# Optimization experiments

Hardware: AMD Instinct MI355X
Metric: run time of the kernel (lower is better)

## Reference

```python
import jax, jax.numpy as jnp
import numpy as np
import math

D = 1024
H = 16

def setup_inputs() -> dict:
    key = jax.random.key(0)
    ks = jax.random.split(key, 8)
    N, X, T = 2, 1024, 4096
    s = 1.0 / math.sqrt(D)
    return {
        "previous_output": jax.random.normal(ks[0], (N, X, D), jnp.float32),
        "context": jax.random.normal(ks[1], (N, T, D), jnp.float32),
        "Wq": jax.random.normal(ks[2], (D, D), jnp.float32) * s,
        "bq": jnp.zeros((D,), jnp.float32),
        "Wk": jax.random.normal(ks[3], (D, D), jnp.float32) * s,
        "bk": jnp.zeros((D,), jnp.float32),
        "Wv": jax.random.normal(ks[4], (D, D), jnp.float32) * s,
        "bv": jnp.zeros((D,), jnp.float32),
    }

def reference(previous_output, context, Wq, bq, Wk, bk, Wv, bv):
    N, X, _ = previous_output.shape
    T = context.shape[1]
    hd = D // H
    # linear projections (torch Linear: x @ W.T + b)
    q = (previous_output @ Wq.T + bq).reshape(N, X, H, hd).transpose(0, 2, 1, 3)  # (N,H,X,hd)
    k = (context @ Wk.T + bk).reshape(N, T, H, hd).transpose(0, 2, 1, 3)          # (N,H,T,hd)
    v = (context @ Wv.T + bv).reshape(N, T, H, hd).transpose(0, 2, 1, 3)          # (N,H,T,hd)
    scores = jnp.einsum('nhxd,nhtd->nhxt', q, k) / jnp.sqrt(jnp.float32(hd))       # (N,H,X,T)
    attn = jax.nn.softmax(scores, axis=-1)
    out = jnp.einsum('nhxt,nhtd->nhxd', attn, v)                                   # (N,H,X,hd)
    return out.transpose(0, 2, 1, 3).reshape(N, X, D)
```

## Files before the change

kernel.cpp:

```cpp
#include <hip/hip_runtime.h>

typedef __bf16 bf16_t;
typedef __bf16 bf16x8 __attribute__((ext_vector_type(8)));
typedef __bf16 bf16x4 __attribute__((ext_vector_type(4)));
typedef float f32x4 __attribute__((ext_vector_type(4)));

#define D_MODEL 1024
#define NHEAD 16
#define HD 64
#define XLEN 1024
#define TLEN 4096
#define NBATCH 2
#define CEXP 0.18033688011112042f

typedef __attribute__((address_space(3))) bf16_t lds_bf16;
typedef const __attribute__((address_space(1))) bf16_t glb_bf16;

#define MEMFENCE() asm volatile("" ::: "memory")

__global__ __launch_bounds__(256) void convert5(const float* __restrict__ prev, const float* __restrict__ ctx,
                                                const float* __restrict__ wq, const float* __restrict__ wk,
                                                const float* __restrict__ wv,
                                                bf16_t* __restrict__ prev_b, bf16_t* __restrict__ ctx_b,
                                                bf16_t* __restrict__ wq_b, bf16_t* __restrict__ wk_b,
                                                bf16_t* __restrict__ wv_b) {
    int b = blockIdx.x;
    const float* src; bf16_t* dst; int lb;
    if (b < 256)       { src = prev; dst = prev_b; lb = b; }
    else if (b < 1280) { src = ctx;  dst = ctx_b;  lb = b - 256; }
    else if (b < 1408) { src = wq;   dst = wq_b;   lb = b - 1280; }
    else if (b < 1536) { src = wk;   dst = wk_b;   lb = b - 1408; }
    else               { src = wv;   dst = wv_b;   lb = b - 1536; }
    const int base = lb * 8192 + threadIdx.x * 4;
#pragma unroll
    for (int i = 0; i < 8; ++i) {
        const int off = base + i * 1024;
        f32x4 f = *(const f32x4*)(src + off);
        bf16x4 h;
        h[0] = (bf16_t)f[0]; h[1] = (bf16_t)f[1]; h[2] = (bf16_t)f[2]; h[3] = (bf16_t)f[3];
        *(bf16x4*)(dst + off) = h;
    }
}

template<int MF>
__device__ __forceinline__ void gemm_core(const bf16_t* __restrict__ Xa,
                                          const bf16_t* __restrict__ Wb,
                                          int m0, int n0, char* smem,
                                          f32x4 (&acc)[MF][4]) {
    const int tid  = threadIdx.x;
    const int w    = tid >> 6;
    const int lane = tid & 63;
    const int q4   = lane >> 4;
    const int c    = lane & 15;
    const int wm   = w >> 2;
    const int wn   = w & 3;

    constexpr int ABYTES = MF * 4096;
    constexpr int BUFSZ  = ABYTES + 32768;
    constexpr int AI     = MF / 4;
    constexpr int NT     = 16;

#pragma unroll
    for (int i = 0; i < MF; ++i)
#pragma unroll
        for (int j = 0; j < 4; ++j) acc[i][j] = (f32x4){0.f, 0.f, 0.f, 0.f};

    const int xp = ((lane & 3) * 16) ^ (((lane >> 5) & 1) << 5);
    const char* gA = (const char*)Xa + ((size_t)(m0 + w * 16 + (lane >> 2)) << 11) + xp;
    const char* gB = (const char*)Wb + ((size_t)(n0 + w * 16 + (lane >> 2)) << 11) + xp;
    char* lw = smem + w * 1024;

    const int fo = c * 64 + ((q4 * 16) ^ (((c >> 3) & 1) << 5));

#pragma unroll
    for (int i = 0; i < AI; ++i)
#pragma unroll
        for (int k = 0; k < 2; ++k)
            __builtin_amdgcn_global_load_lds((glb_bf16*)(gA + (size_t)i * 262144 + k * 64),
                                             (lds_bf16*)(lw + k * (MF * 2048) + i * 8192), 16, 0, 0);
#pragma unroll
    for (int i = 0; i < 2; ++i)
#pragma unroll
        for (int k = 0; k < 2; ++k)
            __builtin_amdgcn_global_load_lds((glb_bf16*)(gB + (size_t)i * 262144 + k * 64),
                                             (lds_bf16*)(lw + ABYTES + k * 16384 + i * 8192), 16, 0, 0);
    MEMFENCE();

#pragma unroll 1
    for (int t = 0; t < NT; ++t) {
        asm volatile("s_waitcnt vmcnt(0)" ::: "memory");
        __builtin_amdgcn_s_barrier();
        MEMFENCE();

        if (t + 1 < NT) {
            char* pb = lw + ((t + 1) & 1) * BUFSZ;
            const size_t tk = (size_t)(t + 1) * 128;
#pragma unroll
            for (int i = 0; i < AI; ++i)
#pragma unroll
                for (int k = 0; k < 2; ++k)
                    __builtin_amdgcn_global_load_lds((glb_bf16*)(gA + (size_t)i * 262144 + tk + k * 64),
                                                     (lds_bf16*)(pb + k * (MF * 2048) + i * 8192), 16, 0, 0);
#pragma unroll
            for (int i = 0; i < 2; ++i)
#pragma unroll
                for (int k = 0; k < 2; ++k)
                    __builtin_amdgcn_global_load_lds((glb_bf16*)(gB + (size_t)i * 262144 + tk + k * 64),
                                                     (lds_bf16*)(pb + ABYTES + k * 16384 + i * 8192), 16, 0, 0);
        }

        const char* cb = smem + (t & 1) * BUFSZ;
#pragma unroll
        for (int kk = 0; kk < 2; ++kk) {
            bf16x8 bfrag[4];
#pragma unroll
            for (int ni = 0; ni < 4; ++ni)
                bfrag[ni] = *(const bf16x8*)(cb + ABYTES + kk * 16384 + (wn * 4 + ni) * 1024 + fo);
            bf16x8 afrag[MF / 2];
#pragma unroll
            for (int mi = 0; mi < MF / 2; ++mi)
                afrag[mi] = *(const bf16x8*)(cb + kk * (MF * 2048) + (wm * MF + mi) * 1024 + fo);
            __builtin_amdgcn_s_setprio(1);
#pragma unroll
            for (int mi = 0; mi < MF / 2; ++mi)
#pragma unroll
                for (int ni = 0; ni < 4; ++ni)
                    acc[mi][ni] = __builtin_amdgcn_mfma_f32_16x16x32_bf16(afrag[mi], bfrag[ni], acc[mi][ni], 0, 0, 0);
            __builtin_amdgcn_s_setprio(0);

            bf16x8 afrag2[MF / 2];
#pragma unroll
            for (int mi = 0; mi < MF / 2; ++mi)
                afrag2[mi] = *(const bf16x8*)(cb + kk * (MF * 2048) + (wm * MF + MF / 2 + mi) * 1024 + fo);
            __builtin_amdgcn_s_setprio(1);
#pragma unroll
            for (int mi = 0; mi < MF / 2; ++mi)
#pragma unroll
                for (int ni = 0; ni < 4; ++ni)
                    acc[MF / 2 + mi][ni] = __builtin_amdgcn_mfma_f32_16x16x32_bf16(afrag2[mi], bfrag[ni], acc[MF / 2 + mi][ni], 0, 0, 0);
            __builtin_amdgcn_s_setprio(0);
            MEMFENCE();
        }
    }
}

__global__ __launch_bounds__(512, 2) void gemm_fused2(
    const bf16_t* __restrict__ Xq, const bf16_t* __restrict__ Xc,
    const bf16_t* __restrict__ wq, const bf16_t* __restrict__ wk, const bf16_t* __restrict__ wv,
    const float* __restrict__ bq, const float* __restrict__ bk, const float* __restrict__ bv,
    bf16_t* __restrict__ Qh, bf16_t* __restrict__ Kh, bf16_t* __restrict__ Vt) {
    __shared__ __align__(16) char smem[131072];
    const int bid  = blockIdx.x;
    const int tid  = threadIdx.x;
    const int w    = tid >> 6;
    const int lane = tid & 63;
    const int q4   = lane >> 4;
    const int c    = lane & 15;
    const int wm   = w >> 2;
    const int wn   = w & 3;
    (void)w;

    if (bid >= 64) {
        const int b     = bid - 64;
        const int r     = b & 7;
        const int j     = (b >> 3) & 7;
        const int mhi   = b >> 6;
        const int vmode = j >> 2;
        const int n0    = (j & 3) * 256;
        const int m0    = (mhi * 8 + r) * 256;
        const bf16_t* W   = vmode ? wv : wk;
        const float* bias = vmode ? bv : bk;

        const int Nw = n0 + wn * 64;
        float bz[4];
#pragma unroll
        for (int ni = 0; ni < 4; ++ni) bz[ni] = bias[Nw + ni * 16 + c];
        MEMFENCE();

        f32x4 acc[8][4];
        gemm_core<8>(Xc, W, m0, n0, smem, acc);

        const int Mw = m0 + wm * 128;
        const int headbase = Nw >> 6;
        if (vmode == 0) {
#pragma unroll
            for (int mi = 0; mi < 8; ++mi) {
                const int mrow = Mw + mi * 16 + q4 * 4;
                const int nb2 = mrow >> 12, pos = mrow & 4095;
                bf16_t* ob = Kh + ((size_t)(nb2 * NHEAD + headbase) * TLEN + pos) * HD;
#pragma unroll
                for (int ni = 0; ni < 4; ++ni) {
                    const int d = ni * 16 + c;
#pragma unroll
                    for (int r2 = 0; r2 < 4; ++r2)
                        ob[(size_t)r2 * HD + d] = (bf16_t)(acc[mi][ni][r2] + bz[ni]);
                }
            }
        } else {
#pragma unroll
            for (int mi = 0; mi < 8; ++mi) {
                const int mrow = Mw + mi * 16 + q4 * 4;
                const int nb2 = mrow >> 12, pos = mrow & 4095;
                const int lin = (pos & ~31) + ((pos >> 2) & 3) * 8 + ((pos >> 4) & 1) * 4;
#pragma unroll
                for (int ni = 0; ni < 4; ++ni) {
                    const int d = ni * 16 + c;
                    bf16x4 v4;
#pragma unroll
                    for (int r2 = 0; r2 < 4; ++r2) v4[r2] = (bf16_t)(acc[mi][ni][r2] + bz[ni]);
                    *(bf16x4*)(Vt + ((size_t)(nb2 * NHEAD + headbase) * HD + d) * TLEN + lin) = v4;
                }
            }
        }
    } else {
        const int b  = bid;
        const int m0 = (b >> 2) * 128;
        const int n0 = (b & 3) * 256;

        const int Nw = n0 + wn * 64;
        float bz[4];
#pragma unroll
        for (int ni = 0; ni < 4; ++ni) bz[ni] = bq[Nw + ni * 16 + c];
        MEMFENCE();

        f32x4 acc[4][4];
        gemm_core<4>(Xq, wq, m0, n0, smem, acc);

        const int Mw = m0 + wm * 64;
        const int headbase = Nw >> 6;
#pragma unroll
        for (int mi = 0; mi < 4; ++mi) {
            const int mrow = Mw + mi * 16 + q4 * 4;
            const int nb2 = mrow >> 10, pos = mrow & 1023;
            bf16_t* ob = Qh + ((size_t)(nb2 * NHEAD + headbase) * XLEN + pos) * HD;
#pragma unroll
            for (int ni = 0; ni < 4; ++ni) {
                const int d = ni * 16 + c;
#pragma unroll
                for (int r2 = 0; r2 < 4; ++r2)
                    ob[(size_t)r2 * HD + d] = (bf16_t)((acc[mi][ni][r2] + bz[ni]) * CEXP);
            }
        }
    }
}

__global__ __launch_bounds__(256, 4) void attn_kernel(const bf16_t* __restrict__ Qh,
                                                      const bf16_t* __restrict__ Kh,
                                                      const bf16_t* __restrict__ Vt,
                                                      bf16_t* __restrict__ Opart,
                                                      float* __restrict__ Lpart) {
    __shared__ __align__(16) char smem[32768];

    const int tid  = threadIdx.x;
    const int lane = tid & 63;
    const int w    = tid >> 6;
    const int q4   = lane >> 4;
    const int c    = lane & 15;

    const int bid = blockIdx.x;
    const int xcd = bid & 7;
    const int seq = bid >> 3;
    const int tq  = seq & 3;
    const int xb  = (seq >> 2) & 7;
    const int g   = seq >> 5;
    const int nh  = g * 8 + xcd;
    const int xw  = xb * 128 + w * 32;

    const bf16_t* __restrict__ Kb = Kh + (size_t)nh * TLEN * HD;
    const bf16_t* __restrict__ Vb = Vt + (size_t)nh * HD * TLEN;

    bf16x8 qa[2][2];
#pragma unroll
    for (int mi = 0; mi < 2; ++mi) {
        const bf16_t* qr = Qh + ((size_t)nh * XLEN + xw + mi * 16 + c) * HD + q4 * 8;
        qa[mi][0] = *(const bf16x8*)(qr);
        qa[mi][1] = *(const bf16x8*)(qr + 32);
    }

    const int sRow0 = tid >> 3,  sRow1 = 32 + (tid >> 3);
    const int sCh   = tid & 7;
    const int kCol0 = ((sCh ^ (sRow0 & 7)) * 8);
    const int kCol1 = ((sCh ^ (sRow1 & 7)) * 8);

    const int ofs0 = c * 128 + ((q4 ^ (c & 7)) * 16);
    const int ofs1 = c * 128 + (((4 + q4) ^ (c & 7)) * 16);

    f32x4 o[2][4];
#pragma unroll
    for (int i = 0; i < 2; ++i)
#pragma unroll
        for (int j = 0; j < 4; ++j) o[i][j] = (f32x4){0.f, 0.f, 0.f, 0.f};
    f32x4 lacc[2];
    lacc[0] = (f32x4){0.f, 0.f, 0.f, 0.f};
    lacc[1] = (f32x4){0.f, 0.f, 0.f, 0.f};

    bf16x8 ones8;
#pragma unroll
    for (int j = 0; j < 8; ++j) ones8[j] = (bf16_t)1.0f;

    const int t0base = tq * (TLEN / 4);

    {
        bf16_t* base = (bf16_t*)smem;
        __builtin_amdgcn_global_load_lds((glb_bf16*)(Kb + (size_t)(t0base + sRow0) * HD + kCol0), (lds_bf16*)(base + w * 512), 16, 0, 0);
        __builtin_amdgcn_global_load_lds((glb_bf16*)(Kb + (size_t)(t0base + sRow1) * HD + kCol1), (lds_bf16*)(base + 2048 + w * 512), 16, 0, 0);
        __builtin_amdgcn_global_load_lds((glb_bf16*)(Vb + (size_t)sRow0 * TLEN + t0base + kCol0), (lds_bf16*)(base + 4096 + w * 512), 16, 0, 0);
        __builtin_amdgcn_global_load_lds((glb_bf16*)(Vb + (size_t)sRow1 * TLEN + t0base + kCol1), (lds_bf16*)(base + 6144 + w * 512), 16, 0, 0);
    }

    for (int s = 0; s < 16; ++s) {
        __syncthreads();
        if (s < 15) {
            const int t1 = t0base + (s + 1) * 64;
            bf16_t* base = (bf16_t*)smem + ((s + 1) & 1) * 8192;
            __builtin_amdgcn_global_load_lds((glb_bf16*)(Kb + (size_t)(t1 + sRow0) * HD + kCol0), (lds_bf16*)(base + w * 512), 16, 0, 0);
            __builtin_amdgcn_global_load_lds((glb_bf16*)(Kb + (size_t)(t1 + sRow1) * HD + kCol1), (lds_bf16*)(base + 2048 + w * 512), 16, 0, 0);
            __builtin_amdgcn_global_load_lds((glb_bf16*)(Vb + (size_t)sRow0 * TLEN + t1 + kCol0), (lds_bf16*)(base + 4096 + w * 512), 16, 0, 0);
            __builtin_amdgcn_global_load_lds((glb_bf16*)(Vb + (size_t)sRow1 * TLEN + t1 + kCol1), (lds_bf16*)(base + 6144 + w * 512), 16, 0, 0);
        }

        const char* KtB = smem + (s & 1) * 16384;
        const char* VsB = KtB + 8192;
#pragma unroll
        for (int g32 = 0; g32 < 2; ++g32) {
            bf16x8 p8[2];
#pragma unroll
            for (int tt = 0; tt < 2; ++tt) {
                const int rofs = g32 * 4096 + tt * 2048;
                bf16x8 kb0 = *(const bf16x8*)(KtB + rofs + ofs0);
                bf16x8 kb1 = *(const bf16x8*)(KtB + rofs + ofs1);
#pragma unroll
                for (int mi = 0; mi < 2; ++mi) {
                    f32x4 sv = (f32x4){0.f, 0.f, 0.f, 0.f};
                    sv = __builtin_amdgcn_mfma_f32_16x16x32_bf16(kb0, qa[mi][0], sv, 0, 0, 0);
                    sv = __builtin_amdgcn_mfma_f32_16x16x32_bf16(kb1, qa[mi][1], sv, 0, 0, 0);
#pragma unroll
                    for (int r = 0; r < 4; ++r)
                        p8[mi][tt * 4 + r] = (bf16_t)__builtin_exp2f(sv[r]);
                }
            }
            const int vsel = g32 ? ofs1 : ofs0;
            bf16x8 va[4];
#pragma unroll
            for (int dt = 0; dt < 4; ++dt)
                va[dt] = *(const bf16x8*)(VsB + vsel + dt * 2048);
#pragma unroll
            for (int mi = 0; mi < 2; ++mi) {
#pragma unroll
                for (int dt = 0; dt < 4; ++dt)
                    o[mi][dt] = __builtin_amdgcn_mfma_f32_16x16x32_bf16(va[dt], p8[mi], o[mi][dt], 0, 0, 0);
                lacc[mi] = __builtin_amdgcn_mfma_f32_16x16x32_bf16(ones8, p8[mi], lacc[mi], 0, 0, 0);
            }
        }
    }

    __syncthreads();
    bf16_t* Ob = (bf16_t*)smem;
    float*  Lb = (float*)(smem + 16896);
#pragma unroll
    for (int mi = 0; mi < 2; ++mi) {
        if (q4 == 0) Lb[w * 32 + mi * 16 + c] = lacc[mi][0];
#pragma unroll
        for (int dt = 0; dt < 4; ++dt)
#pragma unroll
            for (int r = 0; r < 4; ++r)
                Ob[w * 2112 + (dt * 16 + q4 * 4 + r) * 33 + mi * 16 + c] = (bf16_t)o[mi][dt][r];
    }
    {
        const int lr = lane >> 1;
        const int dh = lane & 1;
        bf16x8 out4[4];
#pragma unroll
        for (int j2 = 0; j2 < 4; ++j2)
#pragma unroll
            for (int e = 0; e < 8; ++e)
                out4[j2][e] = Ob[w * 2112 + (dh * 32 + j2 * 8 + e) * 33 + lr];
        const size_t pair = (size_t)nh * XLEN + xw + lr;
        bf16_t* op = Opart + (pair * 4 + tq) * HD + dh * 32;
#pragma unroll
        for (int j2 = 0; j2 < 4; ++j2)
            *(bf16x8*)(op + j2 * 8) = out4[j2];
        if (dh == 0) Lpart[pair * 4 + tq] = Lb[w * 32 + lr];
    }
}

__global__ __launch_bounds__(256) void attn_merge(const bf16_t* __restrict__ Opart,
                                                  const float* __restrict__ Lpart,
                                                  float* __restrict__ Out) {
    const int u    = blockIdx.x * 256 + threadIdx.x;
    const int pair = u >> 3;
    const int d0   = (u & 7) * 8;
    const int nh   = pair >> 10;
    const int x    = pair & 1023;
    const int n    = nh >> 4;
    const int h    = nh & 15;

    float l = 0.f;
    float s[8];
#pragma unroll
    for (int j = 0; j < 8; ++j) s[j] = 0.f;
#pragma unroll
    for (int tqi = 0; tqi < 4; ++tqi) {
        l += Lpart[pair * 4 + tqi];
        bf16x8 v = *(const bf16x8*)(Opart + ((size_t)pair * 4 + tqi) * HD + d0);
#pragma unroll
        for (int j = 0; j < 8; ++j) s[j] += (float)v[j];
    }
    const float inv = 1.0f / l;
    f32x4 v0, v1;
#pragma unroll
    for (int j = 0; j < 4; ++j) { v0[j] = s[j] * inv; v1[j] = s[4 + j] * inv; }
    float* op = Out + ((size_t)(n * XLEN + x)) * D_MODEL + h * HD + d0;
    *(f32x4*)(op)     = v0;
    *(f32x4*)(op + 4) = v1;
}

extern "C" void kernel_launch(void* const* d_in, const int* in_sizes, int n_in,
                              void* d_out, int out_size, void* d_ws, size_t ws_size,
                              hipStream_t stream) {
    (void)in_sizes; (void)n_in; (void)out_size; (void)ws_size;
    const float* prev = (const float*)d_in[0];
    const float* ctx  = (const float*)d_in[1];
    const float* Wq   = (const float*)d_in[2];
    const float* bq   = (const float*)d_in[3];
    const float* Wk   = (const float*)d_in[4];
    const float* bk   = (const float*)d_in[5];
    const float* Wv   = (const float*)d_in[6];
    const float* bv   = (const float*)d_in[7];

    const size_t MiB = 1024 * 1024;
    char* ws = (char*)d_ws;
    bf16_t* prev_b = (bf16_t*)(ws);
    bf16_t* ctx_b  = (bf16_t*)(ws + 4 * MiB);
    bf16_t* wq_b   = (bf16_t*)(ws + 20 * MiB);
    bf16_t* wk_b   = (bf16_t*)(ws + 22 * MiB);
    bf16_t* wv_b   = (bf16_t*)(ws + 24 * MiB);
    bf16_t* Qh     = (bf16_t*)(ws + 26 * MiB);
    bf16_t* Kh     = (bf16_t*)(ws + 30 * MiB);
    bf16_t* Vt     = (bf16_t*)(ws + 46 * MiB);
    bf16_t* Opart  = ctx_b;
    float*  Lpart  = (float*)prev_b;

    convert5<<<1664, 256, 0, stream>>>(prev, ctx, Wq, Wk, Wv, prev_b, ctx_b, wq_b, wk_b, wv_b);
    gemm_fused2<<<320, 512, 0, stream>>>(prev_b, ctx_b, wq_b, wk_b, wv_b, bq, bk, bv, Qh, Kh, Vt);
    attn_kernel<<<1024, 256, 0, stream>>>(Qh, Kh, Vt, Opart, Lpart);
    attn_merge<<<1024, 256, 0, stream>>>(Opart, Lpart, (float*)d_out);
}
```

Measured before the change: 202.1 us.

## Split attention over eight key chunks with atomic accumulation and last-block merge

The attention kernel now splits the key/value sequence into eight chunks instead of four and doubles the grid. Partial outputs and row sums are accumulated in fp32 with global atomic adds, not written as bf16 partials. A per-tile counter lets the last-arriving block normalise and write the final output, which removes the separate merge kernel. This raises parallelism and drops one launch, but adds a memset of the accumulation buffers and a large volume of contended atomic traffic.

```diff
diff --git a/kernel.cpp b/kernel.cpp
--- a/kernel.cpp
+++ b/kernel.cpp
@@ -247,8 +247,10 @@
 __global__ __launch_bounds__(256, 4) void attn_kernel(const bf16_t* __restrict__ Qh,
                                                       const bf16_t* __restrict__ Kh,
                                                       const bf16_t* __restrict__ Vt,
-                                                      bf16_t* __restrict__ Opart,
-                                                      float* __restrict__ Lpart) {
+                                                      float* __restrict__ Osum,
+                                                      float* __restrict__ Lsum,
+                                                      int* __restrict__ cnt,
+                                                      float* __restrict__ Out) {
     __shared__ __align__(16) char smem[32768];
 
     const int tid  = threadIdx.x;
@@ -260,9 +262,9 @@
     const int bid = blockIdx.x;
     const int xcd = bid & 7;
     const int seq = bid >> 3;
-    const int tq  = seq & 3;
-    const int xb  = (seq >> 2) & 7;
-    const int g   = seq >> 5;
+    const int tq  = seq & 7;
+    const int xb  = (seq >> 3) & 7;
+    const int g   = seq >> 6;
     const int nh  = g * 8 + xcd;
     const int xw  = xb * 128 + w * 32;
 
@@ -298,7 +300,8 @@
 #pragma unroll
     for (int j = 0; j < 8; ++j) ones8[j] = (bf16_t)1.0f;
 
-    const int t0base = tq * (TLEN / 4);
+    const int t0base = tq * (TLEN / 8);
+    const int NS = 8;
 
     {
         bf16_t* base = (bf16_t*)smem;
@@ -308,9 +311,9 @@
         __builtin_amdgcn_global_load_lds((glb_bf16*)(Vb + (size_t)sRow1 * TLEN + t0base + kCol1), (lds_bf16*)(base + 6144 + w * 512), 16, 0, 0);
     }
 
-    for (int s = 0; s < 16; ++s) {
+    for (int s = 0; s < NS; ++s) {
         __syncthreads();
-        if (s < 15) {
+        if (s < NS - 1) {
             const int t1 = t0base + (s + 1) * 64;
             bf16_t* base = (bf16_t*)smem + ((s + 1) & 1) * 8192;
             __builtin_amdgcn_global_load_lds((glb_bf16*)(Kb + (size_t)(t1 + sRow0) * HD + kCol0), (lds_bf16*)(base + w * 512), 16, 0, 0);
@@ -354,65 +357,46 @@
         }
     }
 
+    const int nhx = nh * XLEN;
+#pragma unroll
+    for (int mi = 0; mi < 2; ++mi) {
+        const int x = xw + mi * 16 + c;
+        float* obase = Osum + ((size_t)(nhx + x)) * HD;
+#pragma unroll
+        for (int dt = 0; dt < 4; ++dt)
+#pragma unroll
+            for (int r = 0; r < 4; ++r)
+                unsafeAtomicAdd(obase + dt * 16 + q4 * 4 + r, o[mi][dt][r]);
+        if (q4 == 0) unsafeAtomicAdd(Lsum + nhx + x, lacc[mi][0]);
+    }
+    __threadfence();
     __syncthreads();
-    bf16_t* Ob = (bf16_t*)smem;
-    float*  Lb = (float*)(smem + 16896);
-#pragma unroll
-    for (int mi = 0; mi < 2; ++mi) {
-        if (q4 == 0) Lb[w * 32 + mi * 16 + c] = lacc[mi][0];
-#pragma unroll
-        for (int dt = 0; dt < 4; ++dt)
-#pragma unroll
-            for (int r = 0; r < 4; ++r)
-                Ob[w * 2112 + (dt * 16 + q4 * 4 + r) * 33 + mi * 16 + c] = (bf16_t)o[mi][dt][r];
-    }
-    {
-        const int lr = lane >> 1;
-        const int dh = lane & 1;
-        bf16x8 out4[4];
-#pragma unroll
-        for (int j2 = 0; j2 < 4; ++j2)
-#pragma unroll
-            for (int e = 0; e < 8; ++e)
-                out4[j2][e] = Ob[w * 2112 + (dh * 32 + j2 * 8 + e) * 33 + lr];
-        const size_t pair = (size_t)nh * XLEN + xw + lr;
-        bf16_t* op = Opart + (pair * 4 + tq) * HD + dh * 32;
-#pragma unroll
-        for (int j2 = 0; j2 < 4; ++j2)
-            *(bf16x8*)(op + j2 * 8) = out4[j2];
-        if (dh == 0) Lpart[pair * 4 + tq] = Lb[w * 32 + lr];
-    }
-}
-
-__global__ __launch_bounds__(256) void attn_merge(const bf16_t* __restrict__ Opart,
-                                                  const float* __restrict__ Lpart,
-                                                  float* __restrict__ Out) {
-    const int u    = blockIdx.x * 256 + threadIdx.x;
-    const int pair = u >> 3;
-    const int d0   = (u & 7) * 8;
-    const int nh   = pair >> 10;
-    const int x    = pair & 1023;
-    const int n    = nh >> 4;
-    const int h    = nh & 15;
-
-    float l = 0.f;
-    float s[8];
-#pragma unroll
-    for (int j = 0; j < 8; ++j) s[j] = 0.f;
-#pragma unroll
-    for (int tqi = 0; tqi < 4; ++tqi) {
-        l += Lpart[pair * 4 + tqi];
-        bf16x8 v = *(const bf16x8*)(Opart + ((size_t)pair * 4 + tqi) * HD + d0);
-#pragma unroll
-        for (int j = 0; j < 8; ++j) s[j] += (float)v[j];
-    }
-    const float inv = 1.0f / l;
-    f32x4 v0, v1;
-#pragma unroll
-    for (int j = 0; j < 4; ++j) { v0[j] = s[j] * inv; v1[j] = s[4 + j] * inv; }
-    float* op = Out + ((size_t)(n * XLEN + x)) * D_MODEL + h * HD + d0;
-    *(f32x4*)(op)     = v0;
-    *(f32x4*)(op + 4) = v1;
+
+    int* flag = (int*)smem;
+    if (tid == 0) {
+        const int old = atomicAdd(cnt + (nh * 8 + xb), 1);
+        *flag = (old == 7) ? 1 : 0;
+    }
+    __syncthreads();
+
+    if (*flag) {
+        const int row = tid >> 1;
+        const int d0  = (tid & 1) * 32;
+        const int x   = xb * 128 + row;
+        const float l = unsafeAtomicAdd(Lsum + nhx + x, 0.0f);
+        const float inv = 1.0f / l;
+        float* osrc = Osum + ((size_t)(nhx + x)) * HD + d0;
+        const int n = nh >> 4, h = nh & 15;
+        float* op = Out + ((size_t)(n * XLEN + x)) * D_MODEL + h * HD + d0;
+#pragma unroll
+        for (int j = 0; j < 8; ++j) {
+            f32x4 v;
+#pragma unroll
+            for (int e = 0; e < 4; ++e)
+                v[e] = unsafeAtomicAdd(osrc + j * 4 + e, 0.0f) * inv;
+            *(f32x4*)(op + j * 4) = v;
+        }
+    }
 }
 
 extern "C" void kernel_launch(void* const* d_in, const int* in_sizes, int n_in,
@@ -438,11 +422,12 @@
     bf16_t* Qh     = (bf16_t*)(ws + 26 * MiB);
     bf16_t* Kh     = (bf16_t*)(ws + 30 * MiB);
     bf16_t* Vt     = (bf16_t*)(ws + 46 * MiB);
-    bf16_t* Opart  = ctx_b;
-    float*  Lpart  = (float*)prev_b;
+    float*  Osum   = (float*)(ws);
+    float*  Lsum   = (float*)(ws + 8 * MiB);
+    int*    cnt    = (int*)(ws + 8 * MiB + 128 * 1024);
 
     convert5<<<1664, 256, 0, stream>>>(prev, ctx, Wq, Wk, Wv, prev_b, ctx_b, wq_b, wk_b, wv_b);
     gemm_fused2<<<320, 512, 0, stream>>>(prev_b, ctx_b, wq_b, wk_b, wv_b, bq, bk, bv, Qh, Kh, Vt);
-    attn_kernel<<<1024, 256, 0, stream>>>(Qh, Kh, Vt, Opart, Lpart);
-    attn_merge<<<1024, 256, 0, stream>>>(Opart, Lpart, (float*)d_out);
+    hipMemsetAsync(ws, 0, 8 * MiB + 132 * 1024, stream);
+    attn_kernel<<<2048, 256, 0, stream>>>(Qh, Kh, Vt, Osum, Lsum, cnt, (float*)d_out);
 }
```

Measured after the change: 604.8 us. 199% more time.

## Add ping-pong pipelined 256x256 GEMM core for K/V projection

Applied to the files above, without the earlier changes.

Adds a new GEMM core for the 256x256 K/V projection tiles. It double-buffers LDS tiles and splits each K-step into four quadrant MFMA phases, issuing the next tile's global-to-LDS loads in stages between barriers with explicit vmcnt waits. The goal is to overlap global memory loads with MFMA work and to cut LDS fragment register pressure. In exchange it adds many more barriers per iteration and relies on hand-tuned wait counts.

```diff
diff --git a/kernel.cpp b/kernel.cpp
--- a/kernel.cpp
+++ b/kernel.cpp
@@ -69,7 +69,6 @@
     const char* gA = (const char*)Xa + ((size_t)(m0 + w * 16 + (lane >> 2)) << 11) + xp;
     const char* gB = (const char*)Wb + ((size_t)(n0 + w * 16 + (lane >> 2)) << 11) + xp;
     char* lw = smem + w * 1024;
-
     const int fo = c * 64 + ((q4 * 16) ^ (((c >> 3) & 1) << 5));
 
 #pragma unroll
@@ -141,6 +140,140 @@
             __builtin_amdgcn_s_setprio(0);
             MEMFENCE();
         }
+    }
+}
+
+__device__ __forceinline__ void gemm_core8(const bf16_t* __restrict__ Xa,
+                                           const bf16_t* __restrict__ Wb,
+                                           int m0, int n0, char* smem,
+                                           f32x4 (&acc)[8][4]) {
+    const int tid  = threadIdx.x;
+    const int w    = tid >> 6;
+    const int lane = tid & 63;
+    const int q4   = lane >> 4;
+    const int c    = lane & 15;
+    const int wm   = w >> 2;
+    const int wn   = w & 3;
+    constexpr int NT = 16;
+
+#pragma unroll
+    for (int i = 0; i < 8; ++i)
+#pragma unroll
+        for (int j = 0; j < 4; ++j) acc[i][j] = (f32x4){0.f, 0.f, 0.f, 0.f};
+
+    const int rr = lane >> 2;
+    const int xp = ((lane & 3) * 16) ^ (((rr >> 3) & 1) << 5);
+    const char* gA = (const char*)Xa + ((size_t)(m0 + (w >> 1) * 16 + rr) << 11) + (w & 1) * 64 + xp;
+    const char* gB = (const char*)Wb + ((size_t)(n0 + (w >> 1) * 16 + rr) << 11) + (w & 1) * 64 + xp;
+
+    const int fo = c * 64 + ((q4 * 16) ^ (((c >> 3) & 1) << 5));
+
+    auto STAGE = [&](int tile, int j) {
+        const size_t kb = (size_t)tile * 128;
+        const char* g = ((j < 2) ? gA : gB) + (size_t)(j & 1) * 262144 + kb;
+        char* l = smem + (tile & 1) * 65536 + ((j < 2) ? 0 : 32768) + (j & 1) * 16384 + w * 1024;
+        __builtin_amdgcn_global_load_lds((glb_bf16*)(g),          (lds_bf16*)(l),        16, 0, 0);
+        __builtin_amdgcn_global_load_lds((glb_bf16*)(g + 131072), (lds_bf16*)(l + 8192), 16, 0, 0);
+    };
+
+    STAGE(0, 0); STAGE(0, 1); STAGE(0, 2); STAGE(0, 3); STAGE(1, 0);
+    MEMFENCE();
+    asm volatile("s_waitcnt vmcnt(2)" ::: "memory");
+    __builtin_amdgcn_s_barrier();
+    MEMFENCE();
+
+#pragma unroll 1
+    for (int t = 0; t < NT; ++t) {
+        const char* cb = smem + (t & 1) * 65536;
+        const char* Ab = cb + wm * 16384;
+        const char* Bb = cb + 32768 + (wn >> 1) * 16384 + (wn & 1) * 8192;
+
+        bf16x8 a[4][2], b0[2][2], b1[2][2];
+
+#pragma unroll
+        for (int mi = 0; mi < 4; ++mi)
+#pragma unroll
+            for (int kh = 0; kh < 2; ++kh)
+                a[mi][kh] = *(const bf16x8*)(Ab + (mi * 2 + kh) * 1024 + fo);
+#pragma unroll
+        for (int ni = 0; ni < 2; ++ni)
+#pragma unroll
+            for (int kh = 0; kh < 2; ++kh)
+                b0[ni][kh] = *(const bf16x8*)(Bb + (ni * 2 + kh) * 1024 + fo);
+        if (t + 1 < NT) STAGE(t + 1, 1);
+        __builtin_amdgcn_s_barrier();
+        MEMFENCE();
+        __builtin_amdgcn_s_setprio(1);
+#pragma unroll
+        for (int mi = 0; mi < 4; ++mi)
+#pragma unroll
+            for (int ni = 0; ni < 2; ++ni)
+#pragma unroll
+                for (int kh = 0; kh < 2; ++kh)
+                    acc[mi][ni] = __builtin_amdgcn_mfma_f32_16x16x32_bf16(a[mi][kh], b0[ni][kh], acc[mi][ni], 0, 0, 0);
+        __builtin_amdgcn_s_setprio(0);
+        MEMFENCE();
+        __builtin_amdgcn_s_barrier();
+
+#pragma unroll
+        for (int ni = 0; ni < 2; ++ni)
+#pragma unroll
+            for (int kh = 0; kh < 2; ++kh)
+                b1[ni][kh] = *(const bf16x8*)(Bb + ((2 + ni) * 2 + kh) * 1024 + fo);
+        if (t + 1 < NT) STAGE(t + 1, 2);
+        __builtin_amdgcn_s_barrier();
+        MEMFENCE();
+        __builtin_amdgcn_s_setprio(1);
+#pragma unroll
+        for (int mi = 0; mi < 4; ++mi)
+#pragma unroll
+            for (int ni = 0; ni < 2; ++ni)
+#pragma unroll
+                for (int kh = 0; kh < 2; ++kh)
+                    acc[mi][2 + ni] = __builtin_amdgcn_mfma_f32_16x16x32_bf16(a[mi][kh], b1[ni][kh], acc[mi][2 + ni], 0, 0, 0);
+        __builtin_amdgcn_s_setprio(0);
+        MEMFENCE();
+        __builtin_amdgcn_s_barrier();
+
+#pragma unroll
+        for (int mi = 0; mi < 4; ++mi)
+#pragma unroll
+            for (int kh = 0; kh < 2; ++kh)
+                a[mi][kh] = *(const bf16x8*)(Ab + ((4 + mi) * 2 + kh) * 1024 + fo);
+        if (t + 1 < NT) STAGE(t + 1, 3);
+        __builtin_amdgcn_s_barrier();
+        MEMFENCE();
+        __builtin_amdgcn_s_setprio(1);
+#pragma unroll
+        for (int mi = 0; mi < 4; ++mi)
+#pragma unroll
+            for (int ni = 0; ni < 2; ++ni)
+#pragma unroll
+                for (int kh = 0; kh < 2; ++kh)
+                    acc[4 + mi][ni] = __builtin_amdgcn_mfma_f32_16x16x32_bf16(a[mi][kh], b0[ni][kh], acc[4 + mi][ni], 0, 0, 0);
+        __builtin_amdgcn_s_setprio(0);
+        MEMFENCE();
+        __builtin_amdgcn_s_barrier();
+
+        if (t + 2 < NT) STAGE(t + 2, 0);
+        __builtin_amdgcn_s_barrier();
+        MEMFENCE();
+        __builtin_amdgcn_s_setprio(1);
+#pragma unroll
+        for (int mi = 0; mi < 4; ++mi)
+#pragma unroll
+            for (int ni = 0; ni < 2; ++ni)
+#pragma unroll
+                for (int kh = 0; kh < 2; ++kh)
+                    acc[4 + mi][2 + ni] = __builtin_amdgcn_mfma_f32_16x16x32_bf16(a[mi][kh], b1[ni][kh], acc[4 + mi][2 + ni], 0, 0, 0);
+        __builtin_amdgcn_s_setprio(0);
+        MEMFENCE();
+        if (t + 1 < NT) {
+            if (t + 2 < NT) asm volatile("s_waitcnt vmcnt(2)" ::: "memory");
+            else            asm volatile("s_waitcnt vmcnt(0)" ::: "memory");
+        }
+        __builtin_amdgcn_s_barrier();
+        MEMFENCE();
     }
 }
 
@@ -178,7 +311,7 @@
         MEMFENCE();
 
         f32x4 acc[8][4];
-        gemm_core<8>(Xc, W, m0, n0, smem, acc);
+        gemm_core8(Xc, W, m0, n0, smem, acc);
 
         const int Mw = m0 + wm * 128;
         const int headbase = Nw >> 6;
```

After: 202.6 us. About the same (+0.3%).
